# Kernel optimization log

Hardware: AMD Instinct MI355X
Metric: run time of the kernel (lower is better)

The kernel has to match this reference:

```python
import jax, jax.numpy as jnp
import numpy as np

T_STEPS = 16
B, C, H, W = 16, 128, 32, 32
NUM_THRESHOLDS = 8


def setup_inputs() -> dict:
    key = jax.random.key(0)
    x = jax.random.normal(key, ((T_STEPS + 1) * B, C, H, W), dtype=jnp.float32)
    thresh = jnp.array(1.0, dtype=jnp.float32)
    return {"x": x, "thresh": thresh, "T": T_STEPS}


def reference(x, thresh, T):
    K = NUM_THRESHOLDS
    Bt = x.shape[0] // (T + 1)
    xt = x.reshape((T + 1, Bt) + x.shape[1:])  # [T+1, B, C, H, W]

    # thre_shaped[k] = thresh / 2**k ; threshold for firing = 0.75 * thre_shaped
    thre_vec = thresh / (2.0 ** jnp.arange(K, dtype=x.dtype))  # [K]
    thre_shaped = thre_vec.reshape((K,) + (1,) * xt[0].ndim)    # [K,1,1,1,1]
    thre_threshold = thre_shaped * 0.75

    bias = xt[0]

    def step(carry, inp):
        mem, exp_in, exp_out = carry
        xi, t = inp  # t = 1..T (float)
        mem = mem + xi - bias + exp_in - exp_out
        pos = (mem[None] >= thre_threshold).astype(x.dtype)   # [K,B,C,H,W]
        neg = (mem[None] <= -thre_threshold).astype(x.dtype)
        # pos_true[0]=pos[0]; pos_true[k]=pos[k]-pos[k-1]  (first-fired threshold)
        pos_true = jnp.concatenate([pos[:1], pos[1:] - pos[:-1]], axis=0)
        neg_true = jnp.concatenate([neg[:1], neg[1:] - neg[:-1]], axis=0)
        spike = jnp.sum(thre_shaped * (pos_true - neg_true), axis=0)
        mem = mem - spike
        exp_in = exp_in + (xi - bias) / t
        exp_out = exp_out + spike / t
        return (mem, exp_in, exp_out), spike

    init = (jnp.zeros_like(bias), bias, jnp.zeros_like(bias))
    ts = jnp.arange(1, T + 1, dtype=x.dtype)
    _, spikes = jax.lax.scan(step, init, (xt[1:], ts))

    out = jnp.concatenate([jnp.zeros_like(xt[:1]), spikes], axis=0)
    return out.reshape(x.shape)
```

## Files before the change

kernel.cpp:

```cpp
#include <hip/hip_runtime.h>


#define T_STEPS 16
#define K_THRESH 8

__global__ __launch_bounds__(256) void snn_scan_kernel(
    const float* __restrict__ x,
    const float* __restrict__ thresh_p,
    float* __restrict__ out,
    int N4)
{
    const int i = blockIdx.x * blockDim.x + threadIdx.x;
    if (i >= N4) return;

    const float th = *thresh_p;
    float lev[K_THRESH], thq[K_THRESH];
#pragma unroll
    for (int k = 0; k < K_THRESH; ++k) {
        lev[k] = __builtin_ldexpf(th, -k);
        thq[k] = 0.75f * lev[k];
    }

    const float4* __restrict__ xv = (const float4*)x;
    float4* __restrict__ ov = (float4*)out;

    const float4 b4 = xv[i];
    ov[i] = make_float4(0.f, 0.f, 0.f, 0.f);

    float bias[4] = {b4.x, b4.y, b4.z, b4.w};
    float mem[4]  = {0.f, 0.f, 0.f, 0.f};
    float ein[4]  = {bias[0], bias[1], bias[2], bias[3]};
    float eout[4] = {0.f, 0.f, 0.f, 0.f};

    float4 xi4 = xv[N4 + i];

#pragma unroll
    for (int t = 1; t <= T_STEPS; ++t) {
        const float xi[4] = {xi4.x, xi4.y, xi4.z, xi4.w};
        if (t < T_STEPS) xi4 = xv[(t + 1) * N4 + i];

        const float tf = (float)t;
        float sp[4];
#pragma unroll
        for (int j = 0; j < 4; ++j) {
            float m = (((mem[j] + xi[j]) - bias[j]) + ein[j]) - eout[j];

            const float a = fabsf(m);
            float mag = 0.f;
#pragma unroll
            for (int k = K_THRESH - 1; k >= 0; --k)
                mag = (a >= thq[k]) ? lev[k] : mag;
            const float s = (m >= 0.f) ? mag : -mag;

            m = m - s;
            ein[j]  = ein[j]  + (xi[j] - bias[j]) / tf;
            eout[j] = eout[j] + s / tf;
            mem[j] = m;
            sp[j] = s;
        }
        ov[t * N4 + i] = make_float4(sp[0], sp[1], sp[2], sp[3]);
    }
}

extern "C" void kernel_launch(void* const* d_in, const int* in_sizes, int n_in,
                              void* d_out, int out_size, void* d_ws, size_t ws_size,
                              hipStream_t stream) {
    const float* x       = (const float*)d_in[0];
    const float* thresh  = (const float*)d_in[1];
    float* out = (float*)d_out;

    const int N  = in_sizes[0] / (T_STEPS + 1);
    const int N4 = N / 4;

    const int block = 256;
    const int grid  = (N4 + block - 1) / block;
    snn_scan_kernel<<<grid, block, 0, stream>>>(x, thresh, out, N4);
}
```

Measured before the change: 257.7 us.

## Use float2 per thread, nontemporal stores, and reciprocal-based eout update

Each thread now handles two elements with float2 loads instead of four with float4, which doubles the thread count and adds a min-blocks launch bound meant to raise occupancy. Output stores use nontemporal hints to avoid polluting the cache. The spike is now computed as a scale times the threshold, and the eout update uses a precomputed threshold divided by t, with an exact reciprocal only when t is a power of two. The narrower accesses may lower per-thread bandwidth, and the reworked arithmetic could change rounding slightly.

```diff
diff --git a/kernel.cpp b/kernel.cpp
--- a/kernel.cpp
+++ b/kernel.cpp
@@ -4,75 +4,89 @@
 #define T_STEPS 16
 #define K_THRESH 8
 
-__global__ __launch_bounds__(256) void snn_scan_kernel(
+typedef float v2f __attribute__((ext_vector_type(2)));
+
+__global__ __launch_bounds__(256, 8) void snn_scan_kernel(
     const float* __restrict__ x,
     const float* __restrict__ thresh_p,
     float* __restrict__ out,
-    int N4)
+    int N2)
 {
     const int i = blockIdx.x * blockDim.x + threadIdx.x;
-    if (i >= N4) return;
+    if (i >= N2) return;
 
     const float th = *thresh_p;
-    float lev[K_THRESH], thq[K_THRESH];
+    const float thq0 = 0.75f * th;
+    float thq[K_THRESH];
 #pragma unroll
-    for (int k = 0; k < K_THRESH; ++k) {
-        lev[k] = __builtin_ldexpf(th, -k);
-        thq[k] = 0.75f * lev[k];
+    for (int k = 0; k < K_THRESH; ++k) thq[k] = __builtin_ldexpf(thq0, -k);
+
+    const v2f* __restrict__ xv = (const v2f*)x;
+    v2f* __restrict__ ov = (v2f*)out;
+
+    const v2f b2 = xv[i];
+    {
+        v2f z; z.x = 0.f; z.y = 0.f;
+        __builtin_nontemporal_store(z, ov + i);
     }
 
-    const float4* __restrict__ xv = (const float4*)x;
-    float4* __restrict__ ov = (float4*)out;
+    float mem0 = 0.f, mem1 = 0.f;
+    const float bias0 = b2.x, bias1 = b2.y;
+    float ein0 = bias0, ein1 = bias1;
+    float eout0 = 0.f, eout1 = 0.f;
 
-    const float4 b4 = xv[i];
-    ov[i] = make_float4(0.f, 0.f, 0.f, 0.f);
-
-    float bias[4] = {b4.x, b4.y, b4.z, b4.w};
-    float mem[4]  = {0.f, 0.f, 0.f, 0.f};
-    float ein[4]  = {bias[0], bias[1], bias[2], bias[3]};
-    float eout[4] = {0.f, 0.f, 0.f, 0.f};
-
-    float4 xi4 = xv[N4 + i];
+    v2f xi2 = xv[N2 + i];
 
 #pragma unroll
     for (int t = 1; t <= T_STEPS; ++t) {
-        const float xi[4] = {xi4.x, xi4.y, xi4.z, xi4.w};
-        if (t < T_STEPS) xi4 = xv[(t + 1) * N4 + i];
+        const float xi0 = xi2.x, xi1 = xi2.y;
+        if (t < T_STEPS) xi2 = xv[(t + 1) * N2 + i];
 
-        const float tf = (float)t;
-        float sp[4];
+        const bool tp2 = (t & (t - 1)) == 0;
+        const float rt = 1.0f / (float)t;
+        const float q_t = tp2 ? (th * rt)
+                              : (th / (float)t);
+
+        auto stepj = [&](float& mem, float& ein, float& eout,
+                         float xi, float bias) -> float {
+            const float m = (((mem + xi) - bias) + ein) - eout;
+            const float a = __builtin_fabsf(m);
+            float sc = 0.f;
 #pragma unroll
-        for (int j = 0; j < 4; ++j) {
-            float m = (((mem[j] + xi[j]) - bias[j]) + ein[j]) - eout[j];
+            for (int k = K_THRESH - 1; k >= 0; --k) {
+                const float sck = (float)(1.0 / (double)(1 << k));
+                sc = (a >= thq[k]) ? sck : sc;
+            }
+            const bool pos = (m >= 0.f);
+            const float mag = sc * th;
+            const float s   = pos ? mag : -mag;
+            const float sq  = sc * q_t;
+            mem = m - s;
+            const float d = xi - bias;
+            if (tp2) ein = ein + d * rt;
+            else     ein = ein + d / (float)t;
+            eout = eout + (pos ? sq : -sq);
+            return s;
+        };
 
-            const float a = fabsf(m);
-            float mag = 0.f;
-#pragma unroll
-            for (int k = K_THRESH - 1; k >= 0; --k)
-                mag = (a >= thq[k]) ? lev[k] : mag;
-            const float s = (m >= 0.f) ? mag : -mag;
-
-            m = m - s;
-            ein[j]  = ein[j]  + (xi[j] - bias[j]) / tf;
-            eout[j] = eout[j] + s / tf;
-            mem[j] = m;
-            sp[j] = s;
-        }
-        ov[t * N4 + i] = make_float4(sp[0], sp[1], sp[2], sp[3]);
+        v2f sp;
+        sp.x = stepj(mem0, ein0, eout0, xi0, bias0);
+        sp.y = stepj(mem1, ein1, eout1, xi1, bias1);
+        __builtin_nontemporal_store(sp, ov + t * N2 + i);
     }
 }
 
 extern "C" void kernel_launch(void* const* d_in, const int* in_sizes, int n_in,
                               void* d_out, int out_size, void* d_ws, size_t ws_size,
                               hipStream_t stream) {
-    const float* x       = (const float*)d_in[0];
-    const float* thresh  = (const float*)d_in[1];
+    const float* x      = (const float*)d_in[0];
+    const float* thresh = (const float*)d_in[1];
     float* out = (float*)d_out;
 
     const int N  = in_sizes[0] / (T_STEPS + 1);
-    const int N4 = N / 4;
+    const int N2 = N / 2;
 
     const int block = 256;
-    const int grid  = (N4 + block - 1) / block;
-    snn_scan_kernel<<<grid, block, 0, stream>>>(x, thresh, out, N4);
+    const int grid  = (N2 + block - 1) / block;
+    snn_scan_kernel<<<grid, block, 0, stream>>>(x, thresh, out, N2);
 }
```

Result: faster. 251.4 us (-2.5%).
